# Performance work log

Measured on AMD Instinct MI355X. Metric: run time of the kernel, lower is better.

The kernel has to match this reference:

```python
import jax, jax.numpy as jnp
import numpy as np

B, CIN, N = 4, 128, 4096
CKEY, COUT = 64, 128

def setup_inputs() -> dict:
    key = jax.random.key(0)
    k1, k2, k3, k4 = jax.random.split(key, 4)
    x = jax.random.normal(k1, (B, CIN, N), dtype=jnp.float32)
    # Conv1d(kernel_size=1, bias=False) weights as [out, in] matrices
    Wq = jax.random.normal(k2, (CKEY, CIN), dtype=jnp.float32) * (1.0 / np.sqrt(CIN))
    Wk = jax.random.normal(k3, (CKEY, CIN), dtype=jnp.float32) * (1.0 / np.sqrt(CIN))
    Wv = jax.random.normal(k4, (COUT, CIN), dtype=jnp.float32) * (1.0 / np.sqrt(CIN))
    return {"x": x, "Wq": Wq, "Wk": Wk, "Wv": Wv}

def reference(x, Wq, Wk, Wv):
    # 1x1 conv projections: [B, C, N] -> [B, C', N]
    Q = jnp.einsum('ki,bin->bkn', Wq, x)   # [B, CKEY, N]
    K = jnp.einsum('ki,bin->bkn', Wk, x)   # [B, CKEY, N]
    V = jnp.einsum('oi,bin->bon', Wv, x)   # [B, COUT, N]
    # A = softmax(Q^T K) over last dim -- NOTE: no 1/sqrt(d) scaling, as in original
    scores = jnp.einsum('bkn,bkm->bnm', Q, K)     # [B, N, N]
    A = jax.nn.softmax(scores, axis=2)
    # out = (A @ V^T)^T -> [B, COUT, N]
    out = jnp.einsum('bnm,bom->bon', A, V)
    return out
```

## Files before the change

### kernel.cpp

```cpp
#include <hip/hip_runtime.h>
#include <hip/hip_bf16.h>

#define NN    4096
#define BB    4
#define CIN_  128
#define COUT_ 128

typedef __attribute__((ext_vector_type(8))) short bf16x8;
typedef __attribute__((ext_vector_type(4))) short bf16x4;
typedef __attribute__((ext_vector_type(4))) float f32x4;

#define MFMA16 __builtin_amdgcn_mfma_f32_16x16x32_bf16
#define SWK(row, g) ((((row) << 6)) + ((((g) ^ ((row) & 7))) << 3))

__device__ __forceinline__ float bf2f(short s) {
    union { unsigned int u; float f; } c; c.u = ((unsigned int)(unsigned short)s) << 16; return c.f;
}
__device__ __forceinline__ short f2bf(float f) {
    union { float f; unsigned int u; } c; c.f = f;
    unsigned int r = c.u + 0x7fffu + ((c.u >> 16) & 1u);
    return (short)(r >> 16);
}
__device__ __forceinline__ float fexp2(float x) {
#if __has_builtin(__builtin_amdgcn_exp2f)
    return __builtin_amdgcn_exp2f(x);
#else
    return exp2f(x);
#endif
}
__device__ __forceinline__ unsigned int pack_bf16(float a, float b) {
    union { float f; unsigned int u; } ca, cb; ca.f = a; cb.f = b;
    unsigned int ua = ca.u + 0x8000u, ub = cb.u + 0x8000u;
#if __has_builtin(__builtin_amdgcn_perm)
    return __builtin_amdgcn_perm(ub, ua, 0x07060302u);
#else
    return (ua >> 16) | (ub & 0xffff0000u);
#endif
}

__global__ __launch_bounds__(256) void proj_kernel(const float* __restrict__ x,
                                                   const float* __restrict__ Wq,
                                                   const float* __restrict__ Wk,
                                                   const float* __restrict__ Wv,
                                                   short* __restrict__ Qh, short* __restrict__ Ql,
                                                   short* __restrict__ Kh, short* __restrict__ Kl,
                                                   short* __restrict__ Vb) {
    __shared__ __align__(16) short xsh[16 * 64 * 8];
    __shared__ __align__(16) short xsl[16 * 64 * 8];

    int tid  = threadIdx.x;
    int b    = blockIdx.y;
    int gz   = blockIdx.z;
    int gn0  = blockIdx.x * 64;
    int wave = tid >> 6;
    int lane = tid & 63;
    int quad = lane >> 4;
    int l15  = lane & 15;

    const float* xb = x + (size_t)b * CIN_ * NN + gn0;
#pragma unroll
    for (int rep = 0; rep < 4; ++rep) {
        int slot = rep * 256 + tid;
        int c = slot >> 6, n = slot & 63;
        bf16x8 h8, l8;
#pragma unroll
        for (int j = 0; j < 8; ++j) {
            float f = xb[(c * 8 + j) * NN + n];
            short h = f2bf(f);
            h8[j] = h;
            l8[j] = f2bf(f - bf2f(h));
        }
        *(bf16x8*)(xsh + (c * 64 + n) * 8) = h8;
        *(bf16x8*)(xsl + (c * 64 + n) * 8) = l8;
    }
    __syncthreads();

#pragma unroll
    for (int rr = 0; rr < 2; ++rr) {
        int rg = gz * 8 + rr * 4 + wave;

        const float* wrow;
        float scale = 1.0f;
        if (rg < 4)      { wrow = Wq + (rg * 16 + l15) * CIN_; scale = 1.4426950408889634f; }
        else if (rg < 8) { wrow = Wk + ((rg - 4) * 16 + l15) * CIN_; }
        else             { wrow = Wv + ((rg - 8) * 16 + l15) * CIN_; }

        bf16x8 wh[4], wl[4];
#pragma unroll
        for (int kc = 0; kc < 4; ++kc) {
            const float* wp = wrow + kc * 32 + quad * 8;
#pragma unroll
            for (int j = 0; j < 8; ++j) {
                float w = wp[j] * scale;
                short h = f2bf(w);
                wh[kc][j] = h;
                wl[kc][j] = f2bf(w - bf2f(h));
            }
        }

        f32x4 acc[4];
#pragma unroll
        for (int ct = 0; ct < 4; ++ct) acc[ct] = (f32x4){0.f, 0.f, 0.f, 0.f};

#pragma unroll
        for (int kc = 0; kc < 4; ++kc) {
#pragma unroll
            for (int ct = 0; ct < 4; ++ct) {
                bf16x8 xh = *(const bf16x8*)(xsh + (((kc * 4 + quad) * 64) + ct * 16 + l15) * 8);
                bf16x8 xl = *(const bf16x8*)(xsl + (((kc * 4 + quad) * 64) + ct * 16 + l15) * 8);
                acc[ct] = MFMA16(wh[kc], xh, acc[ct], 0, 0, 0);
                acc[ct] = MFMA16(wh[kc], xl, acc[ct], 0, 0, 0);
                acc[ct] = MFMA16(wl[kc], xh, acc[ct], 0, 0, 0);
            }
        }

        if (rg < 8) {
            short* H = (rg < 4) ? Qh : Kh;
            short* L = (rg < 4) ? Ql : Kl;
            int rb    = (rg < 4) ? rg : (rg - 4);
            int chunk = rb * 2 + (quad >> 1);
            int sub   = (quad & 1) * 4;
#pragma unroll
            for (int ct = 0; ct < 4; ++ct) {
                int n = gn0 + ct * 16 + l15;
                bf16x4 h4, l4;
#pragma unroll
                for (int r = 0; r < 4; ++r) {
                    float f = acc[ct][r];
                    short h = f2bf(f);
                    h4[r] = h;
                    l4[r] = f2bf(f - bf2f(h));
                }
                *(bf16x4*)(H + (((b * 8 + chunk) * NN) + n) * 8 + sub) = h4;
                *(bf16x4*)(L + (((b * 8 + chunk) * NN) + n) * 8 + sub) = l4;
            }
        } else {
            int o0 = rg * 16 + quad * 4 - 128;
#pragma unroll
            for (int ct = 0; ct < 4; ++ct) {
                int n = gn0 + ct * 16 + l15;
#pragma unroll
                for (int r = 0; r < 4; ++r)
                    Vb[((size_t)(b * COUT_ + o0 + r)) * NN + n] = f2bf(acc[ct][r]);
            }
        }
    }
}

__global__ __launch_bounds__(256, 2) void flash_kernel(const short* __restrict__ Qh,
                                                       const short* __restrict__ Ql,
                                                       const short* __restrict__ Kh,
                                                       const short* __restrict__ Kl,
                                                       const short* __restrict__ Vb,
                                                       float* __restrict__ outp,
                                                       float* __restrict__ lsum,
                                                       int S, int direct) {
    __shared__ __align__(16) short VT[128 * 64];

    int tid  = threadIdx.x;
    int bx   = blockIdx.x;
    int b    = bx / S;
    int s    = bx - b * S;
    int qt   = blockIdx.y;
    int wave = tid >> 6;
    int lane = tid & 63;
    int quad = lane >> 4;
    int l15  = lane & 15;

    int nq0 = qt * 128 + wave * 32 + l15;
    bf16x8 qh0[2], qh1[2], ql0[2], ql1[2];
#pragma unroll
    for (int u = 0; u < 2; ++u) {
        int nq = nq0 + u * 16;
        qh0[u] = *(const bf16x8*)(Qh + (((b * 8 + quad)     * NN) + nq) * 8);
        qh1[u] = *(const bf16x8*)(Qh + (((b * 8 + 4 + quad) * NN) + nq) * 8);
        ql0[u] = *(const bf16x8*)(Ql + (((b * 8 + quad)     * NN) + nq) * 8);
        ql1[u] = *(const bf16x8*)(Ql + (((b * 8 + 4 + quad) * NN) + nq) * 8);
    }

    f32x4 O[2][8];
#pragma unroll
    for (int u = 0; u < 2; ++u)
#pragma unroll
        for (int f = 0; f < 8; ++f) O[u][f] = (f32x4){0.f, 0.f, 0.f, 0.f};
    float lp[2] = {0.f, 0.f};

    int vrow = tid & 127, vc0 = (tid >> 7) * 4;
    int sl0 = (quad & 1) * 32 + l15;
    int sl1 = sl0 + 16;
    int fsel = quad >> 1;

    int KPS   = NN / S;
    int kb    = s * KPS;
    int iters = KPS / 64;

    const short* KhB = Kh + (size_t)b * 8 * NN * 8;
    const short* KlB = Kl + (size_t)b * 8 * NN * 8;
    const short* VbB = Vb + (size_t)b * COUT_ * NN;

    bf16x8 nv[4];
#pragma unroll
    for (int q = 0; q < 4; ++q)
        nv[q] = *(const bf16x8*)(VbB + (size_t)vrow * NN + kb + (vc0 + q) * 8);

    for (int it = 0; it < iters; ++it) {
        bf16x8 kh0[4], kh1[4], kl0[4], kl1[4];
#pragma unroll
        for (int f = 0; f < 4; ++f) {
            int row = kb + f * 16 + l15;
            kh0[f] = *(const bf16x8*)(KhB + ((quad       * NN) + row) * 8);
            kh1[f] = *(const bf16x8*)(KhB + (((4 + quad) * NN) + row) * 8);
            kl0[f] = *(const bf16x8*)(KlB + ((quad       * NN) + row) * 8);
            kl1[f] = *(const bf16x8*)(KlB + (((4 + quad) * NN) + row) * 8);
        }

#pragma unroll
        for (int q = 0; q < 4; ++q)
            *(bf16x8*)(VT + SWK(vrow, vc0 + q)) = nv[q];
        __syncthreads();

        if (it + 1 < iters) {
            int nb = kb + 64;
#pragma unroll
            for (int q = 0; q < 4; ++q)
                nv[q] = *(const bf16x8*)(VbB + (size_t)vrow * NN + nb + (vc0 + q) * 8);
        }

        f32x4 sA[2][4];
#pragma unroll
        for (int f = 0; f < 4; ++f) {
#pragma unroll
            for (int u = 0; u < 2; ++u) {
                f32x4 acc = (f32x4){0.f, 0.f, 0.f, 0.f};
                acc = MFMA16(kh0[f], qh0[u], acc, 0, 0, 0);
                acc = MFMA16(kh1[f], qh1[u], acc, 0, 0, 0);
                acc = MFMA16(kl0[f], qh0[u], acc, 0, 0, 0);
                acc = MFMA16(kl1[f], qh1[u], acc, 0, 0, 0);
                acc = MFMA16(kh0[f], ql0[u], acc, 0, 0, 0);
                acc = MFMA16(kh1[f], ql1[u], acc, 0, 0, 0);
                sA[u][f] = acc;
            }
        }

        unsigned int pw[2][4][2];
#pragma unroll
        for (int u = 0; u < 2; ++u) {
#pragma unroll
            for (int f = 0; f < 4; ++f) {
                float p0 = fexp2(sA[u][f][0]);
                float p1 = fexp2(sA[u][f][1]);
                float p2 = fexp2(sA[u][f][2]);
                float p3 = fexp2(sA[u][f][3]);
                lp[u] += (p0 + p1) + (p2 + p3);
                pw[u][f][0] = pack_bf16(p0, p1);
                pw[u][f][1] = pack_bf16(p2, p3);
            }
        }

#pragma unroll
        for (int g = 0; g < 2; ++g) {
            union { int i[4]; bf16x8 v; } pb[2];
#pragma unroll
            for (int u = 0; u < 2; ++u) {
                int a0 = __shfl((int)pw[u][g * 2][0],     sl0, 64);
                int a1 = __shfl((int)pw[u][g * 2][1],     sl0, 64);
                int a2 = __shfl((int)pw[u][g * 2][0],     sl1, 64);
                int a3 = __shfl((int)pw[u][g * 2][1],     sl1, 64);
                int b0 = __shfl((int)pw[u][g * 2 + 1][0], sl0, 64);
                int b1 = __shfl((int)pw[u][g * 2 + 1][1], sl0, 64);
                int b2 = __shfl((int)pw[u][g * 2 + 1][0], sl1, 64);
                int b3 = __shfl((int)pw[u][g * 2 + 1][1], sl1, 64);
                pb[u].i[0] = fsel ? b0 : a0;
                pb[u].i[1] = fsel ? b1 : a1;
                pb[u].i[2] = fsel ? b2 : a2;
                pb[u].i[3] = fsel ? b3 : a3;
            }
#pragma unroll
            for (int f8 = 0; f8 < 8; ++f8) {
                bf16x8 vA = *(const bf16x8*)(VT + SWK(f8 * 16 + l15, g * 4 + quad));
                O[0][f8] = MFMA16(vA, pb[0].v, O[0][f8], 0, 0, 0);
                O[1][f8] = MFMA16(vA, pb[1].v, O[1][f8], 0, 0, 0);
            }
        }
        __syncthreads();
        kb += 64;
    }

#pragma unroll
    for (int u = 0; u < 2; ++u) {
        lp[u] += __shfl_xor(lp[u], 16, 64);
        lp[u] += __shfl_xor(lp[u], 32, 64);
    }

#pragma unroll
    for (int u = 0; u < 2; ++u) {
        int n = nq0 + u * 16;
        if (direct) {
            float inv = 1.f / lp[u];
#pragma unroll
            for (int f8 = 0; f8 < 8; ++f8)
#pragma unroll
                for (int r = 0; r < 4; ++r) {
                    int o = f8 * 16 + quad * 4 + r;
                    outp[((size_t)(b * COUT_ + o)) * NN + n] = O[u][f8][r] * inv;
                }
        } else {
#pragma unroll
            for (int f8 = 0; f8 < 8; ++f8)
#pragma unroll
                for (int r = 0; r < 4; ++r) {
                    int o = f8 * 16 + quad * 4 + r;
                    outp[((size_t)((b * S + s) * COUT_ + o)) * NN + n] = O[u][f8][r];
                }
            if (quad == 0) lsum[(b * S + s) * NN + n] = lp[u];
        }
    }
}

__global__ __launch_bounds__(256, 4) void merge_kernel(const float* __restrict__ Opart,
                                                       const float* __restrict__ lsum,
                                                       float* __restrict__ out, int S) {
    int idx = blockIdx.x * 256 + threadIdx.x;
    int n0  = (idx & (NN / 4 - 1)) * 4;
    int rest = idx >> 10;
    int o = rest & (COUT_ - 1);
    int b = rest >> 7;

    f32x4 den = (f32x4){0.f, 0.f, 0.f, 0.f};
    f32x4 acc = (f32x4){0.f, 0.f, 0.f, 0.f};
    for (int s = 0; s < S; ++s) {
        f32x4 l  = *(const f32x4*)(lsum + (b * S + s) * NN + n0);
        f32x4 ov = *(const f32x4*)(Opart + ((size_t)((b * S + s) * COUT_ + o)) * NN + n0);
#pragma unroll
        for (int j = 0; j < 4; ++j) {
            den[j] += l[j];
            acc[j] += ov[j];
        }
    }
    f32x4 res;
#pragma unroll
    for (int j = 0; j < 4; ++j) res[j] = acc[j] / den[j];
    *(f32x4*)(out + ((size_t)(b * COUT_ + o)) * NN + n0) = res;
}

extern "C" void kernel_launch(void* const* d_in, const int* in_sizes, int n_in,
                              void* d_out, int out_size, void* d_ws, size_t ws_size,
                              hipStream_t stream) {
    const float* x  = (const float*)d_in[0];
    const float* Wq = (const float*)d_in[1];
    const float* Wk = (const float*)d_in[2];
    const float* Wv = (const float*)d_in[3];

    char* ws = (char*)d_ws;
    short* Qh = (short*)ws;
    short* Ql = Qh + 1048576;
    short* Kh = Ql + 1048576;
    short* Kl = Kh + 1048576;
    short* Vb = Kl + 1048576;
    size_t base = 4ull * 2097152 + 4194304;
    const size_t MLSZ  = (size_t)BB * NN * 4;
    const size_t OPART = 8388608;

    int S;
    if      (ws_size >= base + 4 * (MLSZ + OPART)) S = 4;
    else if (ws_size >= base + 2 * (MLSZ + OPART)) S = 2;
    else                                           S = 1;
    int direct = (S == 1);

    float* lsum  = (float*)(ws + base);
    float* Opart = (float*)(ws + base + (size_t)S * MLSZ);

    proj_kernel<<<dim3(NN / 64, BB, 2), 256, 0, stream>>>(x, Wq, Wk, Wv, Qh, Ql, Kh, Kl, Vb);
    flash_kernel<<<dim3(BB * S, NN / 128), 256, 0, stream>>>(
        Qh, Ql, Kh, Kl, Vb, direct ? (float*)d_out : Opart, lsum, S, direct);
    if (!direct)
        merge_kernel<<<BB * COUT_ * NN / 4 / 256, 256, 0, stream>>>(Opart, lsum, (float*)d_out, S);
}
```

Baseline: 128.1 us.

## Transpose P via per-wave LDS buffer and split projection grid over more blocks

```diff
diff --git a/kernel.cpp b/kernel.cpp
--- a/kernel.cpp
+++ b/kernel.cpp
@@ -9,6 +9,7 @@
 typedef __attribute__((ext_vector_type(8))) short bf16x8;
 typedef __attribute__((ext_vector_type(4))) short bf16x4;
 typedef __attribute__((ext_vector_type(4))) float f32x4;
+typedef __attribute__((ext_vector_type(2))) int   i32x2;
 
 #define MFMA16 __builtin_amdgcn_mfma_f32_16x16x32_bf16
 #define SWK(row, g) ((((row) << 6)) + ((((g) ^ ((row) & 7))) << 3))
@@ -75,74 +76,71 @@
     }
     __syncthreads();
 
-#pragma unroll
-    for (int rr = 0; rr < 2; ++rr) {
-        int rg = gz * 8 + rr * 4 + wave;
-
-        const float* wrow;
-        float scale = 1.0f;
-        if (rg < 4)      { wrow = Wq + (rg * 16 + l15) * CIN_; scale = 1.4426950408889634f; }
-        else if (rg < 8) { wrow = Wk + ((rg - 4) * 16 + l15) * CIN_; }
-        else             { wrow = Wv + ((rg - 8) * 16 + l15) * CIN_; }
-
-        bf16x8 wh[4], wl[4];
-#pragma unroll
-        for (int kc = 0; kc < 4; ++kc) {
-            const float* wp = wrow + kc * 32 + quad * 8;
-#pragma unroll
-            for (int j = 0; j < 8; ++j) {
-                float w = wp[j] * scale;
-                short h = f2bf(w);
-                wh[kc][j] = h;
-                wl[kc][j] = f2bf(w - bf2f(h));
+    int rg = gz * 4 + wave;
+
+    const float* wrow;
+    float scale = 1.0f;
+    if (rg < 4)      { wrow = Wq + (rg * 16 + l15) * CIN_; scale = 1.4426950408889634f; }
+    else if (rg < 8) { wrow = Wk + ((rg - 4) * 16 + l15) * CIN_; }
+    else             { wrow = Wv + ((rg - 8) * 16 + l15) * CIN_; }
+
+    bf16x8 wh[4], wl[4];
+#pragma unroll
+    for (int kc = 0; kc < 4; ++kc) {
+        const float* wp = wrow + kc * 32 + quad * 8;
+#pragma unroll
+        for (int j = 0; j < 8; ++j) {
+            float w = wp[j] * scale;
+            short h = f2bf(w);
+            wh[kc][j] = h;
+            wl[kc][j] = f2bf(w - bf2f(h));
+        }
+    }
+
+    f32x4 acc[4];
+#pragma unroll
+    for (int ct = 0; ct < 4; ++ct) acc[ct] = (f32x4){0.f, 0.f, 0.f, 0.f};
+
+#pragma unroll
+    for (int kc = 0; kc < 4; ++kc) {
+#pragma unroll
+        for (int ct = 0; ct < 4; ++ct) {
+            bf16x8 xh = *(const bf16x8*)(xsh + (((kc * 4 + quad) * 64) + ct * 16 + l15) * 8);
+            bf16x8 xl = *(const bf16x8*)(xsl + (((kc * 4 + quad) * 64) + ct * 16 + l15) * 8);
+            acc[ct] = MFMA16(wh[kc], xh, acc[ct], 0, 0, 0);
+            acc[ct] = MFMA16(wh[kc], xl, acc[ct], 0, 0, 0);
+            acc[ct] = MFMA16(wl[kc], xh, acc[ct], 0, 0, 0);
+        }
+    }
+
+    if (rg < 8) {
+        short* H = (rg < 4) ? Qh : Kh;
+        short* L = (rg < 4) ? Ql : Kl;
+        int rb    = (rg < 4) ? rg : (rg - 4);
+        int chunk = rb * 2 + (quad >> 1);
+        int sub   = (quad & 1) * 4;
+#pragma unroll
+        for (int ct = 0; ct < 4; ++ct) {
+            int n = gn0 + ct * 16 + l15;
+            bf16x4 h4, l4;
+#pragma unroll
+            for (int r = 0; r < 4; ++r) {
+                float f = acc[ct][r];
+                short h = f2bf(f);
+                h4[r] = h;
+                l4[r] = f2bf(f - bf2f(h));
             }
-        }
-
-        f32x4 acc[4];
-#pragma unroll
-        for (int ct = 0; ct < 4; ++ct) acc[ct] = (f32x4){0.f, 0.f, 0.f, 0.f};
-
-#pragma unroll
-        for (int kc = 0; kc < 4; ++kc) {
-#pragma unroll
-            for (int ct = 0; ct < 4; ++ct) {
-                bf16x8 xh = *(const bf16x8*)(xsh + (((kc * 4 + quad) * 64) + ct * 16 + l15) * 8);
-                bf16x8 xl = *(const bf16x8*)(xsl + (((kc * 4 + quad) * 64) + ct * 16 + l15) * 8);
-                acc[ct] = MFMA16(wh[kc], xh, acc[ct], 0, 0, 0);
-                acc[ct] = MFMA16(wh[kc], xl, acc[ct], 0, 0, 0);
-                acc[ct] = MFMA16(wl[kc], xh, acc[ct], 0, 0, 0);
-            }
-        }
-
-        if (rg < 8) {
-            short* H = (rg < 4) ? Qh : Kh;
-            short* L = (rg < 4) ? Ql : Kl;
-            int rb    = (rg < 4) ? rg : (rg - 4);
-            int chunk = rb * 2 + (quad >> 1);
-            int sub   = (quad & 1) * 4;
-#pragma unroll
-            for (int ct = 0; ct < 4; ++ct) {
-                int n = gn0 + ct * 16 + l15;
-                bf16x4 h4, l4;
-#pragma unroll
-                for (int r = 0; r < 4; ++r) {
-                    float f = acc[ct][r];
-                    short h = f2bf(f);
-                    h4[r] = h;
-                    l4[r] = f2bf(f - bf2f(h));
-                }
-                *(bf16x4*)(H + (((b * 8 + chunk) * NN) + n) * 8 + sub) = h4;
-                *(bf16x4*)(L + (((b * 8 + chunk) * NN) + n) * 8 + sub) = l4;
-            }
-        } else {
-            int o0 = rg * 16 + quad * 4 - 128;
-#pragma unroll
-            for (int ct = 0; ct < 4; ++ct) {
-                int n = gn0 + ct * 16 + l15;
-#pragma unroll
-                for (int r = 0; r < 4; ++r)
-                    Vb[((size_t)(b * COUT_ + o0 + r)) * NN + n] = f2bf(acc[ct][r]);
-            }
+            *(bf16x4*)(H + (((b * 8 + chunk) * NN) + n) * 8 + sub) = h4;
+            *(bf16x4*)(L + (((b * 8 + chunk) * NN) + n) * 8 + sub) = l4;
+        }
+    } else {
+        int o0 = rg * 16 + quad * 4 - 128;
+#pragma unroll
+        for (int ct = 0; ct < 4; ++ct) {
+            int n = gn0 + ct * 16 + l15;
+#pragma unroll
+            for (int r = 0; r < 4; ++r)
+                Vb[((size_t)(b * COUT_ + o0 + r)) * NN + n] = f2bf(acc[ct][r]);
         }
     }
 }
@@ -156,6 +154,7 @@
                                                        float* __restrict__ lsum,
                                                        int S, int direct) {
     __shared__ __align__(16) short VT[128 * 64];
+    __shared__ __align__(16) short PW[4 * 32 * 64];
 
     int tid  = threadIdx.x;
     int bx   = blockIdx.x;
@@ -186,9 +185,7 @@
     float lp[2] = {0.f, 0.f};
 
     int vrow = tid & 127, vc0 = (tid >> 7) * 4;
-    int sl0 = (quad & 1) * 32 + l15;
-    int sl1 = sl0 + 16;
-    int fsel = quad >> 1;
+    short* pwb = PW + wave * 2048;
 
     int KPS   = NN / S;
     int kb    = s * KPS;
@@ -242,9 +239,9 @@
             }
         }
 
-        unsigned int pw[2][4][2];
 #pragma unroll
         for (int u = 0; u < 2; ++u) {
+            int row = u * 16 + l15;
 #pragma unroll
             for (int f = 0; f < 4; ++f) {
                 float p0 = fexp2(sA[u][f][0]);
@@ -252,34 +249,22 @@
                 float p2 = fexp2(sA[u][f][2]);
                 float p3 = fexp2(sA[u][f][3]);
                 lp[u] += (p0 + p1) + (p2 + p3);
-                pw[u][f][0] = pack_bf16(p0, p1);
-                pw[u][f][1] = pack_bf16(p2, p3);
+                unsigned int w0 = pack_bf16(p0, p1);
+                unsigned int w1 = pack_bf16(p2, p3);
+                *(i32x2*)(pwb + SWK(row, f * 2 + (quad >> 1)) + (quad & 1) * 4) =
+                    (i32x2){(int)w0, (int)w1};
             }
         }
 
 #pragma unroll
         for (int g = 0; g < 2; ++g) {
-            union { int i[4]; bf16x8 v; } pb[2];
-#pragma unroll
-            for (int u = 0; u < 2; ++u) {
-                int a0 = __shfl((int)pw[u][g * 2][0],     sl0, 64);
-                int a1 = __shfl((int)pw[u][g * 2][1],     sl0, 64);
-                int a2 = __shfl((int)pw[u][g * 2][0],     sl1, 64);
-                int a3 = __shfl((int)pw[u][g * 2][1],     sl1, 64);
-                int b0 = __shfl((int)pw[u][g * 2 + 1][0], sl0, 64);
-                int b1 = __shfl((int)pw[u][g * 2 + 1][1], sl0, 64);
-                int b2 = __shfl((int)pw[u][g * 2 + 1][0], sl1, 64);
-                int b3 = __shfl((int)pw[u][g * 2 + 1][1], sl1, 64);
-                pb[u].i[0] = fsel ? b0 : a0;
-                pb[u].i[1] = fsel ? b1 : a1;
-                pb[u].i[2] = fsel ? b2 : a2;
-                pb[u].i[3] = fsel ? b3 : a3;
-            }
+            bf16x8 pb0 = *(const bf16x8*)(pwb + SWK(l15,      g * 4 + quad));
+            bf16x8 pb1 = *(const bf16x8*)(pwb + SWK(16 + l15, g * 4 + quad));
 #pragma unroll
             for (int f8 = 0; f8 < 8; ++f8) {
                 bf16x8 vA = *(const bf16x8*)(VT + SWK(f8 * 16 + l15, g * 4 + quad));
-                O[0][f8] = MFMA16(vA, pb[0].v, O[0][f8], 0, 0, 0);
-                O[1][f8] = MFMA16(vA, pb[1].v, O[1][f8], 0, 0, 0);
+                O[0][f8] = MFMA16(vA, pb0, O[0][f8], 0, 0, 0);
+                O[1][f8] = MFMA16(vA, pb1, O[1][f8], 0, 0, 0);
             }
         }
         __syncthreads();
@@ -370,7 +355,7 @@
     float* lsum  = (float*)(ws + base);
     float* Opart = (float*)(ws + base + (size_t)S * MLSZ);
 
-    proj_kernel<<<dim3(NN / 64, BB, 2), 256, 0, stream>>>(x, Wq, Wk, Wv, Qh, Ql, Kh, Kl, Vb);
+    proj_kernel<<<dim3(NN / 64, BB, 4), 256, 0, stream>>>(x, Wq, Wk, Wv, Qh, Ql, Kh, Kl, Vb);
     flash_kernel<<<dim3(BB * S, NN / 128), 256, 0, stream>>>(
         Qh, Ql, Kh, Kl, Vb, direct ? (float*)d_out : Opart, lsum, S, direct);
     if (!direct)
```

Result: faster. 124.0 us (-3.2%).
